# Optimization experiments

Measured on AMD Instinct MI355X. Metric: run time of the kernel, lower is better.

## Reference

```python
import jax, jax.numpy as jnp
import numpy as np

D, H, V, CTX, L = 1024, 16, 50257, 1024, 4
B, S = 2, 1024
DK = D // H
DFF = 4 * D


def layernorm(x, g, b, eps=1e-5):
    mu = jnp.mean(x, axis=-1, keepdims=True)
    var = jnp.var(x, axis=-1, keepdims=True)
    return (x - mu) * jax.lax.rsqrt(var + eps) * g + b


def setup_inputs() -> dict:
    key = jax.random.key(0)
    ks = jax.random.split(key, 20)
    s = 0.02
    inp = {
        'idx': jax.random.randint(ks[0], (B, S), 0, V, dtype=jnp.int32),
        'te': jax.random.normal(ks[1], (V, D), jnp.float32) * s,
        'pe': jax.random.normal(ks[2], (CTX, D), jnp.float32) * s,
        # per-layer stacked params; linear weights stored [in, out]
        'wq': jax.random.normal(ks[3], (L, D, D), jnp.float32) * s,
        'bq': jnp.zeros((L, D), jnp.float32),
        'wk': jax.random.normal(ks[4], (L, D, D), jnp.float32) * s,
        'bk': jnp.zeros((L, D), jnp.float32),
        'wv': jax.random.normal(ks[5], (L, D, D), jnp.float32) * s,
        'bv': jnp.zeros((L, D), jnp.float32),
        'wo': jax.random.normal(ks[6], (L, D, D), jnp.float32) * s,
        'bo': jnp.zeros((L, D), jnp.float32),
        'ln2_g': jnp.ones((L, D), jnp.float32),
        'ln2_b': jnp.zeros((L, D), jnp.float32),
        'w1': jax.random.normal(ks[7], (L, D, DFF), jnp.float32) * s,
        'b1': jnp.zeros((L, DFF), jnp.float32),
        'w2': jax.random.normal(ks[8], (L, DFF, D), jnp.float32) * s,
        'b2': jnp.zeros((L, D), jnp.float32),
        'lnf_g': jnp.ones((D,), jnp.float32),
        'lnf_b': jnp.zeros((D,), jnp.float32),
    }
    return inp


def reference(idx, te, pe, wq, bq, wk, bk, wv, bv, wo, bo,
              ln2_g, ln2_b, w1, b1, w2, b2, lnf_g, lnf_b):
    Bc, Sc = idx.shape
    x = te[idx] + pe[:Sc][None, :, :]  # [B,S,D]
    scale = 1.0 / np.sqrt(DK).astype(np.float32)
    causal = jnp.tril(jnp.ones((Sc, Sc), jnp.bool_))
    neg_inf = jnp.finfo(x.dtype).min
    for l in range(L):
        # NOTE: source passes ln1(x) only as shape carrier; q=k=v=raw x (faithful)
        q = (x @ wq[l] + bq[l]).reshape(Bc, Sc, H, DK)
        k = (x @ wk[l] + bk[l]).reshape(Bc, Sc, H, DK)
        v = (x @ wv[l] + bv[l]).reshape(Bc, Sc, H, DK)
        attn = jnp.einsum('bshd,bthd->bhst', q, k) * scale
        attn = jnp.where(causal[None, None], attn, neg_inf)
        attn = jax.nn.softmax(attn, axis=-1)
        y = jnp.einsum('bhst,bthd->bshd', attn, v).reshape(Bc, Sc, D)
        x = x + (y @ wo[l] + bo[l])
        h = layernorm(x, ln2_g[l], ln2_b[l])
        h = jax.nn.gelu(h @ w1[l] + b1[l], approximate=False) @ w2[l] + b2[l]
        x = x + h
    x = layernorm(x, lnf_g, lnf_b)
    logits = x @ te.T  # weight-tied lm_head
    return logits
```

## Files before the change

kernel.cpp:

```cpp
#include <hip/hip_runtime.h>
#include <hip/hip_bf16.h>
#include <math.h>

#define D_   1024
#define H_   16
#define V_   50257
#define L_   4
#define B_   2
#define S_   1024
#define DK_  64
#define DFF_ 4096
#define NT_  (B_*S_)

using bf16 = __hip_bfloat16;
typedef __attribute__((ext_vector_type(8))) __bf16 bf16x8;
typedef __attribute__((ext_vector_type(4))) float  f32x4;

__device__ __forceinline__ void gload_lds16(const void* g, void* l)
{
    __builtin_amdgcn_global_load_lds(
        (const __attribute__((address_space(1))) unsigned int*)g,
        (__attribute__((address_space(3))) unsigned int*)l, 16, 0, 0);
}

template<int BM, int BN>
__global__ __launch_bounds__(256) void gemm_bt(
    const bf16* __restrict__ A, int lda, long long sA1, long long sA2,
    const bf16* __restrict__ Bm, int ldb, long long sB1, long long sB2,
    const float* __restrict__ bias, float scale,
    const float* __restrict__ Rz, int ldr,
    float* __restrict__ CF, int ldcF, long long sCF1, long long sCF2,
    bf16* __restrict__ CB, int ldcB, long long sCB1, long long sCB2,
    int M, int N, int K, int bz2, int gelu_f, int causal, int swapxy)
{
    int bx = blockIdx.x, by = blockIdx.y;
    if (swapxy) { const int t = bx; bx = by; by = t; }
    const int m0 = by * BM;
    const int n0 = bx * BN;
    if (causal && n0 > m0 + BM - 1) return;

    const int z  = blockIdx.z;
    const int b1 = z / bz2, b2 = z % bz2;
    A  += (long long)b1 * sA1 + (long long)b2 * sA2;
    Bm += (long long)b1 * sB1 + (long long)b2 * sB2;
    const long long cfoff = (long long)b1 * sCF1 + (long long)b2 * sCF2;
    const long long cboff = (long long)b1 * sCB1 + (long long)b2 * sCB2;

    __shared__ __align__(16) bf16 As[BM * 32];
    __shared__ __align__(16) bf16 Bs[BN * 32];

    const int tid  = threadIdx.x;
    const int lane = tid & 63;
    const int wave = tid >> 6;
    const int wm = (wave >> 1) * 64;
    const int wn = (wave & 1) * (BN / 2);
    constexpr int WM = 4;
    constexpr int WN = (BN / 2) / 16;

    f32x4 acc[WM][WN] = {};

    const int lm = lane & 15;
    const int lk = (lane >> 4) * 8;

    const int lrow  = lane >> 2;
    const int lcolb = (lane & 3) * 16;

    constexpr int CA = BM / 16 / 4;
    constexpr int CB_ = BN / 16 / 4;

    for (int k0 = 0; k0 < K; k0 += 32) {
        #pragma unroll
        for (int it = 0; it < CA; it++) {
            const int c = wave + it * 4;
            const char* src = (const char*)(A + (long long)(m0 + c * 16 + lrow) * lda + k0) + lcolb;
            gload_lds16(src, &As[c * 16 * 32]);
        }
        #pragma unroll
        for (int it = 0; it < CB_; it++) {
            const int c = wave + it * 4;
            int rr = n0 + c * 16 + lrow; rr = rr < N ? rr : N - 1;
            const char* src = (const char*)(Bm + (long long)rr * ldb + k0) + lcolb;
            gload_lds16(src, &Bs[c * 16 * 32]);
        }
        __syncthreads();

        bf16x8 af[WM], bfr[WN];
        #pragma unroll
        for (int i = 0; i < WM; i++)
            af[i] = *(const bf16x8*)&As[(wm + i * 16 + lm) * 32 + lk];
        #pragma unroll
        for (int j = 0; j < WN; j++)
            bfr[j] = *(const bf16x8*)&Bs[(wn + j * 16 + lm) * 32 + lk];

        #pragma unroll
        for (int i = 0; i < WM; i++)
            #pragma unroll
            for (int j = 0; j < WN; j++)
                acc[i][j] = __builtin_amdgcn_mfma_f32_16x16x32_bf16(
                    af[i], bfr[j], acc[i][j], 0, 0, 0);
        __syncthreads();
    }

    const int rmb = (lane >> 4) << 2;
    #pragma unroll
    for (int i = 0; i < WM; i++) {
        #pragma unroll
        for (int j = 0; j < WN; j++) {
            const int n = n0 + wn + j * 16 + lm;
            if (n >= N) continue;
            const float bv = bias ? bias[n] : 0.0f;
            #pragma unroll
            for (int r = 0; r < 4; r++) {
                const int m = m0 + wm + i * 16 + rmb + r;
                float v = acc[i][j][r] * scale + bv;
                if (gelu_f) v = 0.5f * v * (1.0f + erff(v * 0.70710678118654752f));
                if (Rz) v += Rz[(long long)m * ldr + n];
                if (CF) CF[cfoff + (long long)m * ldcF + n] = v;
                if (CB) CB[cboff + (long long)m * ldcB + n] = __float2bfloat16(v);
            }
        }
    }
}

__global__ __launch_bounds__(256) void convT(const float* __restrict__ in,
                                             bf16* __restrict__ out, int K, int N)
{
    __shared__ float tile[32][33];
    const int bx = blockIdx.x * 32;
    const int by = blockIdx.y * 32;
    const int tx = threadIdx.x & 31, ty = threadIdx.x >> 5;
    #pragma unroll
    for (int i = 0; i < 32; i += 8)
        tile[ty + i][tx] = in[(long long)(by + ty + i) * N + bx + tx];
    __syncthreads();
    #pragma unroll
    for (int i = 0; i < 32; i += 8)
        out[(long long)(bx + ty + i) * K + by + tx] = __float2bfloat16(tile[tx][ty + i]);
}

__global__ __launch_bounds__(256) void conv_bf16(const float* __restrict__ in,
                                                 bf16* __restrict__ out, long long n)
{
    const long long i = ((long long)blockIdx.x * 256 + threadIdx.x) * 4;
    if (i >= n) return;
    const float4 v = *(const float4*)&in[i];
    union { bf16 h[4]; uint2 u; } o;
    o.h[0] = __float2bfloat16(v.x); o.h[1] = __float2bfloat16(v.y);
    o.h[2] = __float2bfloat16(v.z); o.h[3] = __float2bfloat16(v.w);
    *(uint2*)&out[i] = o.u;
}

__global__ __launch_bounds__(256) void transpose_v(const bf16* __restrict__ v,
                                                   bf16* __restrict__ vT)
{
    __shared__ bf16 tile[32][33];
    const int bh = blockIdx.z;
    const int b = bh >> 4, h = bh & 15;
    const int s0 = blockIdx.x * 32, d0 = blockIdx.y * 32;
    const int tx = threadIdx.x & 31, ty = threadIdx.x >> 5;
    const bf16* src = v + (long long)b * S_ * D_ + h * DK_;
    #pragma unroll
    for (int i = 0; i < 32; i += 8)
        tile[ty + i][tx] = src[(long long)(s0 + ty + i) * D_ + d0 + tx];
    __syncthreads();
    bf16* dst = vT + (long long)bh * DK_ * S_;
    #pragma unroll
    for (int i = 0; i < 32; i += 8)
        dst[(long long)(d0 + ty + i) * S_ + s0 + tx] = tile[tx][ty + i];
}

__global__ __launch_bounds__(64) void embed_kernel(const int* __restrict__ idx,
    const float* __restrict__ te, const float* __restrict__ pe,
    float* __restrict__ x, bf16* __restrict__ xb)
{
    const int t = blockIdx.x;
    const int s = t & (S_ - 1);
    const int id = idx[t];
    const float* tr = te + (long long)id * D_;
    const float* pr = pe + (long long)s * D_;
    float* xr  = x  + (long long)t * D_;
    bf16*  xbr = xb + (long long)t * D_;
    for (int i = threadIdx.x * 4; i < D_; i += 256) {
        const float4 a = *(const float4*)&tr[i];
        const float4 b = *(const float4*)&pr[i];
        const float4 c = {a.x + b.x, a.y + b.y, a.z + b.z, a.w + b.w};
        *(float4*)&xr[i] = c;
        union { bf16 h[4]; uint2 u; } o;
        o.h[0] = __float2bfloat16(c.x); o.h[1] = __float2bfloat16(c.y);
        o.h[2] = __float2bfloat16(c.z); o.h[3] = __float2bfloat16(c.w);
        *(uint2*)&xbr[i] = o.u;
    }
}

__global__ __launch_bounds__(64) void layernorm_kernel(const float* __restrict__ x,
    const float* __restrict__ g, const float* __restrict__ b, bf16* __restrict__ out)
{
    const int row = blockIdx.x;
    const float* xr = x + (long long)row * D_;
    float s = 0.f, ss = 0.f;
    for (int i = threadIdx.x * 4; i < D_; i += 256) {
        const float4 v = *(const float4*)&xr[i];
        s  += v.x + v.y + v.z + v.w;
        ss += v.x * v.x + v.y * v.y + v.z * v.z + v.w * v.w;
    }
    #pragma unroll
    for (int off = 32; off; off >>= 1) {
        s  += __shfl_down(s, off);
        ss += __shfl_down(ss, off);
    }
    s = __shfl(s, 0); ss = __shfl(ss, 0);
    const float mean = s * (1.0f / D_);
    const float var  = ss * (1.0f / D_) - mean * mean;
    const float rstd = rsqrtf(var + 1e-5f);
    bf16* orow = out + (long long)row * D_;
    for (int i = threadIdx.x * 4; i < D_; i += 256) {
        const float4 v = *(const float4*)&xr[i];
        union { bf16 h[4]; uint2 u; } o;
        o.h[0] = __float2bfloat16((v.x - mean) * rstd * g[i]     + b[i]);
        o.h[1] = __float2bfloat16((v.y - mean) * rstd * g[i + 1] + b[i + 1]);
        o.h[2] = __float2bfloat16((v.z - mean) * rstd * g[i + 2] + b[i + 2]);
        o.h[3] = __float2bfloat16((v.w - mean) * rstd * g[i + 3] + b[i + 3]);
        *(uint2*)&orow[i] = o.u;
    }
}

__global__ __launch_bounds__(64) void softmax_kernel(const float* __restrict__ sc,
                                                     bf16* __restrict__ P)
{
    const int sq = blockIdx.x;
    const long long base = ((long long)blockIdx.y * S_ + sq) * S_;
    const float* row = sc + base;
    bf16* prow = P + base;
    const int lane = threadIdx.x;
    const int len = sq + 1;
    float mx = -3.0e38f;
    for (int i = lane; i < len; i += 64) mx = fmaxf(mx, row[i]);
    #pragma unroll
    for (int off = 32; off; off >>= 1) mx = fmaxf(mx, __shfl_down(mx, off));
    mx = __shfl(mx, 0);
    float sum = 0.f;
    for (int i = lane; i < len; i += 64) sum += __expf(row[i] - mx);
    #pragma unroll
    for (int off = 32; off; off >>= 1) sum += __shfl_down(sum, off);
    sum = __shfl(sum, 0);
    const float inv = 1.0f / sum;
    for (int i = lane; i < S_; i += 64) {
        const float pv = (i < len) ? __expf(row[i] - mx) * inv : 0.f;
        prow[i] = __float2bfloat16(pv);
    }
}

__global__ void ws_fail_kernel(float* out) { out[0] = 12345.0f; }

extern "C" void kernel_launch(void* const* d_in, const int* in_sizes, int n_in,
                              void* d_out, int out_size, void* d_ws, size_t ws_size,
                              hipStream_t stream)
{
    const int*   idx  = (const int*)  d_in[0];
    const float* te   = (const float*)d_in[1];
    const float* pe   = (const float*)d_in[2];
    const float* wq   = (const float*)d_in[3];
    const float* bq   = (const float*)d_in[4];
    const float* wk   = (const float*)d_in[5];
    const float* bk   = (const float*)d_in[6];
    const float* wv   = (const float*)d_in[7];
    const float* bv   = (const float*)d_in[8];
    const float* wo   = (const float*)d_in[9];
    const float* bo   = (const float*)d_in[10];
    const float* ln2g = (const float*)d_in[11];
    const float* ln2b = (const float*)d_in[12];
    const float* w1   = (const float*)d_in[13];
    const float* b1   = (const float*)d_in[14];
    const float* w2   = (const float*)d_in[15];
    const float* b2   = (const float*)d_in[16];
    const float* lnfg = (const float*)d_in[17];
    const float* lnfb = (const float*)d_in[18];
    float* logits = (float*)d_out;

    char* p = (char*)d_ws;
    auto alloc = [&](size_t bytes) {
        void* q = p; p += (bytes + 255) & ~(size_t)255; return q;
    };
    float* x   = (float*)alloc((size_t)NT_ * D_ * 4);
    bf16*  xb  = (bf16*) alloc((size_t)NT_ * D_ * 2);
    bf16*  q_  = (bf16*) alloc((size_t)NT_ * D_ * 2);
    bf16*  k_  = (bf16*) alloc((size_t)NT_ * D_ * 2);
    bf16*  v_  = (bf16*) alloc((size_t)NT_ * D_ * 2);
    bf16*  vT  = (bf16*) alloc((size_t)NT_ * D_ * 2);
    bf16*  y_  = (bf16*) alloc((size_t)NT_ * D_ * 2);
    bf16*  hln = (bf16*) alloc((size_t)NT_ * D_ * 2);
    bf16*  h1  = (bf16*) alloc((size_t)NT_ * DFF_ * 2);
    float* sc  = (float*)alloc((size_t)B_ * H_ * S_ * S_ * 4);
    bf16*  P   = (bf16*) alloc((size_t)B_ * H_ * S_ * S_ * 2);
    bf16*  wqT = (bf16*) alloc((size_t)D_ * D_ * 2);
    bf16*  wkT = (bf16*) alloc((size_t)D_ * D_ * 2);
    bf16*  wvT = (bf16*) alloc((size_t)D_ * D_ * 2);
    bf16*  woT = (bf16*) alloc((size_t)D_ * D_ * 2);
    bf16*  w1T = (bf16*) alloc((size_t)D_ * DFF_ * 2);
    bf16*  w2T = (bf16*) alloc((size_t)D_ * DFF_ * 2);
    bf16*  teB = (bf16*) alloc((size_t)V_ * D_ * 2);

    if ((size_t)(p - (char*)d_ws) > ws_size) {
        ws_fail_kernel<<<1, 1, 0, stream>>>(logits);
        return;
    }

    {
        const long long n = (long long)V_ * D_;
        conv_bf16<<<dim3((unsigned)((n / 4 + 255) / 256)), 256, 0, stream>>>(te, teB, n);
    }
    embed_kernel<<<NT_, 64, 0, stream>>>(idx, te, pe, x, xb);

    const long long ZA = (long long)S_ * D_;
    const long long ZS = (long long)S_ * S_;

    for (int l = 0; l < L_; l++) {
        convT<<<dim3(32, 32), 256, 0, stream>>>(wq + (size_t)l * D_ * D_, wqT, D_, D_);
        convT<<<dim3(32, 32), 256, 0, stream>>>(wk + (size_t)l * D_ * D_, wkT, D_, D_);
        convT<<<dim3(32, 32), 256, 0, stream>>>(wv + (size_t)l * D_ * D_, wvT, D_, D_);
        convT<<<dim3(32, 32), 256, 0, stream>>>(wo + (size_t)l * D_ * D_, woT, D_, D_);
        convT<<<dim3(DFF_ / 32, 32), 256, 0, stream>>>(w1 + (size_t)l * D_ * DFF_, w1T, D_, DFF_);
        convT<<<dim3(32, DFF_ / 32), 256, 0, stream>>>(w2 + (size_t)l * DFF_ * D_, w2T, DFF_, D_);

        gemm_bt<128,128><<<dim3(8, 16, 1), 256, 0, stream>>>(
            xb, D_, 0, 0, wqT, D_, 0, 0, bq + l * D_, 1.f, nullptr, 0,
            nullptr, 0, 0, 0, q_, D_, 0, 0, NT_, D_, D_, 1, 0, 0, 0);
        gemm_bt<128,128><<<dim3(8, 16, 1), 256, 0, stream>>>(
            xb, D_, 0, 0, wkT, D_, 0, 0, bk + l * D_, 1.f, nullptr, 0,
            nullptr, 0, 0, 0, k_, D_, 0, 0, NT_, D_, D_, 1, 0, 0, 0);
        gemm_bt<128,128><<<dim3(8, 16, 1), 256, 0, stream>>>(
            xb, D_, 0, 0, wvT, D_, 0, 0, bv + l * D_, 1.f, nullptr, 0,
            nullptr, 0, 0, 0, v_, D_, 0, 0, NT_, D_, D_, 1, 0, 0, 0);

        transpose_v<<<dim3(S_ / 32, DK_ / 32, B_ * H_), 256, 0, stream>>>(v_, vT);

        gemm_bt<128,128><<<dim3(8, 8, B_ * H_), 256, 0, stream>>>(
            q_, D_, ZA, DK_, k_, D_, ZA, DK_, nullptr, 0.125f, nullptr, 0,
            sc, S_, (long long)H_ * ZS, ZS, nullptr, 0, 0, 0,
            S_, S_, DK_, H_, 0, 1, 0);

        softmax_kernel<<<dim3(S_, B_ * H_), 64, 0, stream>>>(sc, P);

        gemm_bt<128,64><<<dim3(1, 8, B_ * H_), 256, 0, stream>>>(
            P, S_, (long long)H_ * ZS, ZS, vT, S_, (long long)H_ * DK_ * S_, (long long)DK_ * S_,
            nullptr, 1.f, nullptr, 0, nullptr, 0, 0, 0,
            y_, D_, ZA, DK_, S_, DK_, S_, H_, 0, 0, 0);

        gemm_bt<128,128><<<dim3(8, 16, 1), 256, 0, stream>>>(
            y_, D_, 0, 0, woT, D_, 0, 0, bo + l * D_, 1.f, x, D_,
            x, D_, 0, 0, nullptr, 0, 0, 0, NT_, D_, D_, 1, 0, 0, 0);

        layernorm_kernel<<<NT_, 64, 0, stream>>>(x, ln2g + l * D_, ln2b + l * D_, hln);

        gemm_bt<128,128><<<dim3(DFF_ / 128, 16, 1), 256, 0, stream>>>(
            hln, D_, 0, 0, w1T, D_, 0, 0, b1 + l * DFF_, 1.f, nullptr, 0,
            nullptr, 0, 0, 0, h1, DFF_, 0, 0, NT_, DFF_, D_, 1, 1, 0, 0);

        gemm_bt<128,128><<<dim3(8, 16, 1), 256, 0, stream>>>(
            h1, DFF_, 0, 0, w2T, DFF_, 0, 0, b2 + l * D_, 1.f, x, D_,
            x, D_, 0, 0, xb, D_, 0, 0, NT_, D_, DFF_, 1, 0, 0, 0);
    }

    layernorm_kernel<<<NT_, 64, 0, stream>>>(x, lnfg, lnfb, hln);

    gemm_bt<128,128><<<dim3(16, (V_ + 127) / 128, 1), 256, 0, stream>>>(
        hln, D_, 0, 0, teB, D_, 0, 0, nullptr, 1.f, nullptr, 0,
        logits, V_, 0, 0, nullptr, 0, 0, 0, NT_, V_, D_, 1, 0, 0, 1);
}
```

Measured before the change: 2.745 ms.

## Fuse QKV projections, clip causal K loop, add XCD-aware rasterization and smaller tiles

Merges the three Q/K/V projection GEMMs into one GEMM over a concatenated weight and bias, writing an interleaved QKV buffer. The P·V GEMM stops its K loop at the causal boundary, and softmax only writes the zero-padded region that the clipped GEMM will read. The lm_head GEMM gets an XCD-aware workgroup remapping to improve L2 locality across the MI355X chiplets. The Wo and W2 GEMMs switch to 64x128 tiles for more workgroups. These cut wasted causal work, launch count and tail effects, at the cost of an extra bias concat kernel and a strided QKV layout.

```diff
diff --git a/kernel.cpp b/kernel.cpp
--- a/kernel.cpp
+++ b/kernel.cpp
@@ -31,10 +31,23 @@
     const float* __restrict__ Rz, int ldr,
     float* __restrict__ CF, int ldcF, long long sCF1, long long sCF2,
     bf16* __restrict__ CB, int ldcB, long long sCB1, long long sCB2,
-    int M, int N, int K, int bz2, int gelu_f, int causal, int swapxy)
+    int M, int N, int K, int bz2, int gelu_f, int causal, int raster, int kclip)
 {
     int bx = blockIdx.x, by = blockIdx.y;
-    if (swapxy) { const int t = bx; bx = by; by = t; }
+    if (raster) {
+        unsigned mi = bx, ni = by;
+        if (raster == 2) {
+            const unsigned nwg = gridDim.x * gridDim.y;
+            const unsigned lin = by * gridDim.x + bx;
+            const unsigned q = nwg >> 3, r = nwg & 7;
+            const unsigned xcd = lin & 7, pos = lin >> 3;
+            const unsigned nid = (xcd < r) ? xcd * (q + 1) + pos
+                                           : r * (q + 1) + (xcd - r) * q + pos;
+            mi = nid % gridDim.x;
+            ni = nid / gridDim.x;
+        }
+        bx = ni; by = mi;
+    }
     const int m0 = by * BM;
     const int n0 = bx * BN;
     if (causal && n0 > m0 + BM - 1) return;
@@ -46,15 +59,18 @@
     const long long cfoff = (long long)b1 * sCF1 + (long long)b2 * sCF2;
     const long long cboff = (long long)b1 * sCB1 + (long long)b2 * sCB2;
 
+    int K_use = K;
+    if (kclip) { const int kk = m0 + BM; K_use = kk < K ? kk : K; }
+
     __shared__ __align__(16) bf16 As[BM * 32];
     __shared__ __align__(16) bf16 Bs[BN * 32];
 
     const int tid  = threadIdx.x;
     const int lane = tid & 63;
     const int wave = tid >> 6;
-    const int wm = (wave >> 1) * 64;
+    const int wm = (wave >> 1) * (BM / 2);
     const int wn = (wave & 1) * (BN / 2);
-    constexpr int WM = 4;
+    constexpr int WM = (BM / 2) / 16;
     constexpr int WN = (BN / 2) / 16;
 
     f32x4 acc[WM][WN] = {};
@@ -65,10 +81,10 @@
     const int lrow  = lane >> 2;
     const int lcolb = (lane & 3) * 16;
 
-    constexpr int CA = BM / 16 / 4;
+    constexpr int CA  = BM / 16 / 4;
     constexpr int CB_ = BN / 16 / 4;
 
-    for (int k0 = 0; k0 < K; k0 += 32) {
+    for (int k0 = 0; k0 < K_use; k0 += 32) {
         #pragma unroll
         for (int it = 0; it < CA; it++) {
             const int c = wave + it * 4;
@@ -150,7 +166,14 @@
     *(uint2*)&out[i] = o.u;
 }
 
-__global__ __launch_bounds__(256) void transpose_v(const bf16* __restrict__ v,
+__global__ __launch_bounds__(256) void concat3(const float* __restrict__ a,
+    const float* __restrict__ b, const float* __restrict__ c, float* __restrict__ o)
+{
+    const int i = blockIdx.x * 256 + threadIdx.x;
+    if (i < D_) { o[i] = a[i]; o[D_ + i] = b[i]; o[2 * D_ + i] = c[i]; }
+}
+
+__global__ __launch_bounds__(256) void transpose_v(const bf16* __restrict__ v, int ldv,
                                                    bf16* __restrict__ vT)
 {
     __shared__ bf16 tile[32][33];
@@ -158,10 +181,10 @@
     const int b = bh >> 4, h = bh & 15;
     const int s0 = blockIdx.x * 32, d0 = blockIdx.y * 32;
     const int tx = threadIdx.x & 31, ty = threadIdx.x >> 5;
-    const bf16* src = v + (long long)b * S_ * D_ + h * DK_;
+    const bf16* src = v + (long long)b * S_ * ldv + h * DK_;
     #pragma unroll
     for (int i = 0; i < 32; i += 8)
-        tile[ty + i][tx] = src[(long long)(s0 + ty + i) * D_ + d0 + tx];
+        tile[ty + i][tx] = src[(long long)(s0 + ty + i) * ldv + d0 + tx];
     __syncthreads();
     bf16* dst = vT + (long long)bh * DK_ * S_;
     #pragma unroll
@@ -233,6 +256,7 @@
     bf16* prow = P + base;
     const int lane = threadIdx.x;
     const int len = sq + 1;
+    const int lim = (sq & ~127) + 128;
     float mx = -3.0e38f;
     for (int i = lane; i < len; i += 64) mx = fmaxf(mx, row[i]);
     #pragma unroll
@@ -244,7 +268,7 @@
     for (int off = 32; off; off >>= 1) sum += __shfl_down(sum, off);
     sum = __shfl(sum, 0);
     const float inv = 1.0f / sum;
-    for (int i = lane; i < S_; i += 64) {
+    for (int i = lane; i < lim; i += 64) {
         const float pv = (i < len) ? __expf(row[i] - mx) * inv : 0.f;
         prow[i] = __float2bfloat16(pv);
     }
@@ -281,38 +305,44 @@
     auto alloc = [&](size_t bytes) {
         void* q = p; p += (bytes + 255) & ~(size_t)255; return q;
     };
-    float* x   = (float*)alloc((size_t)NT_ * D_ * 4);
-    bf16*  xb  = (bf16*) alloc((size_t)NT_ * D_ * 2);
-    bf16*  q_  = (bf16*) alloc((size_t)NT_ * D_ * 2);
-    bf16*  k_  = (bf16*) alloc((size_t)NT_ * D_ * 2);
-    bf16*  v_  = (bf16*) alloc((size_t)NT_ * D_ * 2);
-    bf16*  vT  = (bf16*) alloc((size_t)NT_ * D_ * 2);
-    bf16*  y_  = (bf16*) alloc((size_t)NT_ * D_ * 2);
-    bf16*  hln = (bf16*) alloc((size_t)NT_ * D_ * 2);
-    bf16*  h1  = (bf16*) alloc((size_t)NT_ * DFF_ * 2);
-    float* sc  = (float*)alloc((size_t)B_ * H_ * S_ * S_ * 4);
-    bf16*  P   = (bf16*) alloc((size_t)B_ * H_ * S_ * S_ * 2);
-    bf16*  wqT = (bf16*) alloc((size_t)D_ * D_ * 2);
-    bf16*  wkT = (bf16*) alloc((size_t)D_ * D_ * 2);
-    bf16*  wvT = (bf16*) alloc((size_t)D_ * D_ * 2);
-    bf16*  woT = (bf16*) alloc((size_t)D_ * D_ * 2);
-    bf16*  w1T = (bf16*) alloc((size_t)D_ * DFF_ * 2);
-    bf16*  w2T = (bf16*) alloc((size_t)D_ * DFF_ * 2);
-    bf16*  teB = (bf16*) alloc((size_t)V_ * D_ * 2);
+    float* x    = (float*)alloc((size_t)NT_ * D_ * 4);
+    bf16*  xb   = (bf16*) alloc((size_t)NT_ * D_ * 2);
+    bf16*  qkv  = (bf16*) alloc((size_t)NT_ * 3 * D_ * 2);
+    bf16*  vT   = (bf16*) alloc((size_t)NT_ * D_ * 2);
+    bf16*  y_   = (bf16*) alloc((size_t)NT_ * D_ * 2);
+    bf16*  hln  = (bf16*) alloc((size_t)NT_ * D_ * 2);
+    bf16*  h1   = (bf16*) alloc((size_t)NT_ * DFF_ * 2);
+    float* sc   = (float*)alloc((size_t)B_ * H_ * S_ * S_ * 4);
+    bf16*  P    = (bf16*) alloc((size_t)B_ * H_ * S_ * S_ * 2);
+    bf16*  wqkvT= (bf16*) alloc((size_t)3 * D_ * D_ * 2);
+    bf16*  woT  = (bf16*) alloc((size_t)D_ * D_ * 2);
+    bf16*  w1T  = (bf16*) alloc((size_t)D_ * DFF_ * 2);
+    bf16*  w2T  = (bf16*) alloc((size_t)D_ * DFF_ * 2);
+    bf16*  teB  = (bf16*) alloc((size_t)V_ * D_ * 2);
+    float* bqkv = (float*)alloc((size_t)3 * D_ * 4);
 
     if ((size_t)(p - (char*)d_ws) > ws_size) {
         ws_fail_kernel<<<1, 1, 0, stream>>>(logits);
         return;
     }
 
+    bf16* wqT = wqkvT;
+    bf16* wkT = wqkvT + (size_t)D_ * D_;
+    bf16* wvT = wqkvT + (size_t)2 * D_ * D_;
+    bf16* q_  = qkv;
+    bf16* k_  = qkv + D_;
+    bf16* v_  = qkv + 2 * D_;
+    const int ldq = 3 * D_;
+
     {
         const long long n = (long long)V_ * D_;
         conv_bf16<<<dim3((unsigned)((n / 4 + 255) / 256)), 256, 0, stream>>>(te, teB, n);
     }
     embed_kernel<<<NT_, 64, 0, stream>>>(idx, te, pe, x, xb);
 
-    const long long ZA = (long long)S_ * D_;
-    const long long ZS = (long long)S_ * S_;
+    const long long ZAQ = (long long)S_ * ldq;
+    const long long ZA  = (long long)S_ * D_;
+    const long long ZS  = (long long)S_ * S_;
 
     for (int l = 0; l < L_; l++) {
         convT<<<dim3(32, 32), 256, 0, stream>>>(wq + (size_t)l * D_ * D_, wqT, D_, D_);
@@ -321,49 +351,45 @@
         convT<<<dim3(32, 32), 256, 0, stream>>>(wo + (size_t)l * D_ * D_, woT, D_, D_);
         convT<<<dim3(DFF_ / 32, 32), 256, 0, stream>>>(w1 + (size_t)l * D_ * DFF_, w1T, D_, DFF_);
         convT<<<dim3(32, DFF_ / 32), 256, 0, stream>>>(w2 + (size_t)l * DFF_ * D_, w2T, DFF_, D_);
-
-        gemm_bt<128,128><<<dim3(8, 16, 1), 256, 0, stream>>>(
-            xb, D_, 0, 0, wqT, D_, 0, 0, bq + l * D_, 1.f, nullptr, 0,
-            nullptr, 0, 0, 0, q_, D_, 0, 0, NT_, D_, D_, 1, 0, 0, 0);
-        gemm_bt<128,128><<<dim3(8, 16, 1), 256, 0, stream>>>(
-            xb, D_, 0, 0, wkT, D_, 0, 0, bk + l * D_, 1.f, nullptr, 0,
-            nullptr, 0, 0, 0, k_, D_, 0, 0, NT_, D_, D_, 1, 0, 0, 0);
-        gemm_bt<128,128><<<dim3(8, 16, 1), 256, 0, stream>>>(
-            xb, D_, 0, 0, wvT, D_, 0, 0, bv + l * D_, 1.f, nullptr, 0,
-            nullptr, 0, 0, 0, v_, D_, 0, 0, NT_, D_, D_, 1, 0, 0, 0);
-
-        transpose_v<<<dim3(S_ / 32, DK_ / 32, B_ * H_), 256, 0, stream>>>(v_, vT);
+        concat3<<<dim3(4), 256, 0, stream>>>(bq + (size_t)l * D_, bk + (size_t)l * D_,
+                                             bv + (size_t)l * D_, bqkv);
+
+        gemm_bt<64,128><<<dim3(24, 32, 1), 256, 0, stream>>>(
+            xb, D_, 0, 0, wqkvT, D_, 0, 0, bqkv, 1.f, nullptr, 0,
+            nullptr, 0, 0, 0, qkv, ldq, 0, 0, NT_, 3 * D_, D_, 1, 0, 0, 0, 0);
+
+        transpose_v<<<dim3(S_ / 32, DK_ / 32, B_ * H_), 256, 0, stream>>>(v_, ldq, vT);
 
         gemm_bt<128,128><<<dim3(8, 8, B_ * H_), 256, 0, stream>>>(
-            q_, D_, ZA, DK_, k_, D_, ZA, DK_, nullptr, 0.125f, nullptr, 0,
+            q_, ldq, ZAQ, DK_, k_, ldq, ZAQ, DK_, nullptr, 0.125f, nullptr, 0,
             sc, S_, (long long)H_ * ZS, ZS, nullptr, 0, 0, 0,
-            S_, S_, DK_, H_, 0, 1, 0);
+            S_, S_, DK_, H_, 0, 1, 0, 0);
 
         softmax_kernel<<<dim3(S_, B_ * H_), 64, 0, stream>>>(sc, P);
 
         gemm_bt<128,64><<<dim3(1, 8, B_ * H_), 256, 0, stream>>>(
             P, S_, (long long)H_ * ZS, ZS, vT, S_, (long long)H_ * DK_ * S_, (long long)DK_ * S_,
             nullptr, 1.f, nullptr, 0, nullptr, 0, 0, 0,
-            y_, D_, ZA, DK_, S_, DK_, S_, H_, 0, 0, 0);
-
-        gemm_bt<128,128><<<dim3(8, 16, 1), 256, 0, stream>>>(
+            y_, D_, ZA, DK_, S_, DK_, S_, H_, 0, 0, 0, 1);
+
+        gemm_bt<64,128><<<dim3(8, 32, 1), 256, 0, stream>>>(
             y_, D_, 0, 0, woT, D_, 0, 0, bo + l * D_, 1.f, x, D_,
-            x, D_, 0, 0, nullptr, 0, 0, 0, NT_, D_, D_, 1, 0, 0, 0);
+            x, D_, 0, 0, nullptr, 0, 0, 0, NT_, D_, D_, 1, 0, 0, 0, 0);
 
         layernorm_kernel<<<NT_, 64, 0, stream>>>(x, ln2g + l * D_, ln2b + l * D_, hln);
 
         gemm_bt<128,128><<<dim3(DFF_ / 128, 16, 1), 256, 0, stream>>>(
             hln, D_, 0, 0, w1T, D_, 0, 0, b1 + l * DFF_, 1.f, nullptr, 0,
-            nullptr, 0, 0, 0, h1, DFF_, 0, 0, NT_, DFF_, D_, 1, 1, 0, 0);
-
-        gemm_bt<128,128><<<dim3(8, 16, 1), 256, 0, stream>>>(
+            nullptr, 0, 0, 0, h1, DFF_, 0, 0, NT_, DFF_, D_, 1, 1, 0, 0, 0);
+
+        gemm_bt<64,128><<<dim3(8, 32, 1), 256, 0, stream>>>(
             h1, DFF_, 0, 0, w2T, DFF_, 0, 0, b2 + l * D_, 1.f, x, D_,
-            x, D_, 0, 0, xb, D_, 0, 0, NT_, D_, DFF_, 1, 0, 0, 0);
+            x, D_, 0, 0, xb, D_, 0, 0, NT_, D_, DFF_, 1, 0, 0, 0, 0);
     }
 
     layernorm_kernel<<<NT_, 64, 0, stream>>>(x, lnfg, lnfb, hln);
 
     gemm_bt<128,128><<<dim3(16, (V_ + 127) / 128, 1), 256, 0, stream>>>(
         hln, D_, 0, 0, teB, D_, 0, 0, nullptr, 1.f, nullptr, 0,
-        logits, V_, 0, 0, nullptr, 0, 0, 0, NT_, V_, D_, 1, 0, 0, 1);
-}
+        logits, V_, 0, 0, nullptr, 0, 0, 0, NT_, V_, D_, 1, 0, 0, 2, 0);
+}
```

Result: faster. 2.258 ms (-17.7%).
